# Kernel optimization log

Hardware: AMD Instinct MI355X
Metric: run time of the kernel (lower is better)

## Reference

```python
import jax, jax.numpy as jnp
import numpy as np


def conv(x, w, b=None, pad=1):
    y = jax.lax.conv_general_dilated(x, w, (1, 1), [(pad, pad), (pad, pad)],
                                     dimension_numbers=('NCHW', 'OIHW', 'NCHW'))
    if b is not None:
        y = y + b[None, :, None, None]
    return y


def grid_sample(img, gx, gy):
    # bilinear, zeros padding, align_corners=False (torch F.grid_sample default)
    B, C, H, W = img.shape
    ix = ((gx + 1.0) * W - 1.0) * 0.5
    iy = ((gy + 1.0) * H - 1.0) * 0.5
    x0 = jnp.floor(ix)
    y0 = jnp.floor(iy)

    def gather(xi, yi):
        valid = (xi >= 0) & (xi <= W - 1) & (yi >= 0) & (yi <= H - 1)
        xc = jnp.clip(xi, 0, W - 1).astype(jnp.int32)
        yc = jnp.clip(yi, 0, H - 1).astype(jnp.int32)
        b = jnp.arange(B)[:, None, None]
        return img[b, :, yc, xc] * valid[..., None].astype(img.dtype)  # (B,H,W,C)

    wx1 = ix - x0
    wy1 = iy - y0
    wx0 = 1.0 - wx1
    wy0 = 1.0 - wy1
    out = (gather(x0, y0) * (wx0 * wy0)[..., None]
           + gather(x0 + 1, y0) * (wx1 * wy0)[..., None]
           + gather(x0, y0 + 1) * (wx0 * wy1)[..., None]
           + gather(x0 + 1, y0 + 1) * (wx1 * wy1)[..., None])
    return out.transpose(0, 3, 1, 2)  # (B,C,H,W)


def setup_inputs() -> dict:
    key = jax.random.key(0)
    ks = jax.random.split(key, 32)
    B, H, W, hd = 4, 512, 512, 16
    f = lambda k, shp: jax.random.normal(k, shp, dtype=jnp.float32) * 0.05
    z = lambda n: jnp.zeros((n,), dtype=jnp.float32)
    d = {
        'net': f(ks[0], (B, hd, H, W)),
        'inp': f(ks[1], (B, hd, H, W)),
        'corr': f(ks[2], (B, 3, H, W)),
        'noise': f(ks[3], (B, 3, H, W)),
        # BasicMotionEncoder (channels=3, hidden=32, output_dim=64)
        'wc1': f(ks[4], (32, 3, 3, 3)), 'bc1': z(32),
        'wc2': f(ks[5], (32, 32, 3, 3)), 'bc2': z(32),
        'wf1': f(ks[6], (32, 3, 3, 3)), 'bf1': z(32),
        'wf2': f(ks[7], (32, 32, 3, 3)), 'bf2': z(32),
        'we': f(ks[8], (61, 64, 3, 3)), 'be': z(61),
        # SepConvGRU (hidden_size=16, L=4)
        'loc1_w': f(ks[9], (16, 96, 5, 5)), 'loc1_b': z(16),
        'loc2_w': f(ks[10], (8, 16, 5, 5)), 'loc2_b': z(8),
        'wz': f(ks[11], (16, 144, 3, 3)), 'bz': z(16),
        'wr': f(ks[12], (16, 144, 3, 3)), 'br': z(16),
        'wq': f(ks[13], (16, 96, 3, 3)), 'bq': z(16),
        # CBAM (reduction 16 -> mid=1; bias-free, standard impl)
        'ca_w1': f(ks[14], (1, 16, 1, 1)),
        'ca_w2': f(ks[15], (16, 1, 1, 1)),
        'sa_w': f(ks[16], (1, 2, 7, 7)),
        # FlowHead (input 16, hidden 64, out 3)
        'fh1_w': f(ks[17], (64, 16, 3, 3)), 'fh1_b': z(64),
        'fh2_w': f(ks[18], (3, 64, 3, 3)), 'fh2_b': z(3),
    }
    return d


def reference(net, inp, corr, noise, wc1, bc1, wc2, bc2, wf1, bf1, wf2, bf2, we, be,
              loc1_w, loc1_b, loc2_w, loc2_b, wz, bz, wr, br, wq, bq,
              ca_w1, ca_w2, sa_w, fh1_w, fh1_b, fh2_w, fh2_b):
    # --- BasicMotionEncoder ---
    cor = jax.nn.relu(conv(corr, wc1, bc1, 1))
    cor = jax.nn.relu(conv(cor, wc2, bc2, 1))
    flo = jax.nn.relu(conv(noise, wf1, bf1, 1))
    flo = jax.nn.relu(conv(flo, wf2, bf2, 1))
    mo = jax.nn.relu(conv(jnp.concatenate([cor, flo], 1), we, be, 1))
    motion = jnp.concatenate([mo, noise], 1)  # (B,64,H,W)
    x = jnp.concatenate([inp, motion], 1)     # (B,hd+64,H,W)
    h = net
    B, C, H, W = h.shape
    # --- SepConvGRU ---
    t = jax.nn.leaky_relu(conv(jnp.concatenate([x, h], 1), loc1_w, loc1_b, 2), 0.2)
    flows = conv(t, loc2_w, loc2_b, 2)        # (B,2L,H,W)
    L = flows.shape[1] // 2
    flows = flows.reshape(B, L, 2, H, W)
    xx = jnp.arange(W, dtype=h.dtype)[None, None, :]  # (1,1,W)
    yy = jnp.arange(H, dtype=h.dtype)[None, :, None]  # (1,H,1)

    def warp_one(flow):  # flow: (B,2,H,W); warp h by -flow
        vgx = xx - flow[:, 0]
        vgy = yy - flow[:, 1]
        gx = 2.0 * vgx / max(W - 1, 1) - 1.0
        gy = 2.0 * vgy / max(H - 1, 1) - 1.0
        return grid_sample(h, gx, gy)

    wrapped = jax.vmap(warp_one, in_axes=1, out_axes=1)(flows)  # (B,L,C,H,W)
    wrapped = wrapped.reshape(B, L * C, H, W)
    hx = jnp.concatenate([wrapped, x], 1)     # (B,9*hd,H,W)
    zg = jax.nn.sigmoid(conv(hx, wz, bz, 1))
    rg = jax.nn.sigmoid(conv(hx, wr, br, 1))
    q = jnp.tanh(conv(jnp.concatenate([rg * h, x], 1), wq, bq, 1))
    h = (1.0 - zg) * h + zg * q
    # --- CBAM ---
    avg = h.mean((2, 3), keepdims=True)
    mx = h.max((2, 3), keepdims=True)
    mlp = lambda v: conv(jax.nn.relu(conv(v, ca_w1, None, 0)), ca_w2, None, 0)
    h = h * jax.nn.sigmoid(mlp(avg) + mlp(mx))
    sa = jnp.concatenate([h.mean(1, keepdims=True), h.max(1, keepdims=True)], 1)
    h = h * jax.nn.sigmoid(conv(sa, sa_w, None, 3))
    # --- FlowHead ---
    delta_flow = conv(jax.nn.relu(conv(h, fh1_w, fh1_b, 1)), fh2_w, fh2_b, 1)
    return h, delta_flow
```

## Files before the change

kernel.cpp:

```cpp
#include <hip/hip_runtime.h>
#include <hip/hip_bf16.h>
#include <math.h>

using bf16 = __hip_bfloat16;
typedef __attribute__((ext_vector_type(8))) short short8;
typedef __attribute__((ext_vector_type(4))) float f32x4;

__device__ __forceinline__ float b2f(bf16 v){ return __bfloat162float(v); }
__device__ __forceinline__ bf16 f2b(float v){ return __float2bfloat16(v); }
__device__ __forceinline__ float bs2f(short s){
  union{unsigned u; float f;} x; x.u = ((unsigned)(unsigned short)s)<<16; return x.f;
}
__device__ __forceinline__ float lo16(unsigned u){ union{unsigned x; float f;} v; v.x = u<<16;          return v.f; }
__device__ __forceinline__ float hi16(unsigned u){ union{unsigned x; float f;} v; v.x = u & 0xffff0000u; return v.f; }
__device__ __forceinline__ unsigned cvt_pk_bf16(float lo, float hi){
  unsigned r; asm("v_cvt_pk_bf16_f32 %0, %1, %2" : "=v"(r) : "v"(lo), "v"(hi)); return r;
}
__device__ __forceinline__ float hw_exp2(float x){ float r; asm("v_exp_f32 %0, %1" : "=v"(r) : "v"(x)); return r; }
__device__ __forceinline__ float hw_rcp(float x){ float r; asm("v_rcp_f32 %0, %1" : "=v"(r) : "v"(x)); return r; }
__device__ __forceinline__ float fast_sigmoid(float v){ return hw_rcp(1.f + hw_exp2(v * -1.44269504f)); }
__device__ __forceinline__ float fast_tanh(float v){ return 1.f - 2.f*hw_rcp(1.f + hw_exp2(v * 2.88539008f)); }

template<int A> __device__ __forceinline__ float act_fn(float v){
  if constexpr (A==1) return fmaxf(v, 0.f);
  else if constexpr (A==2) return v > 0.f ? v : 0.2f*v;
  else if constexpr (A==3) return fast_sigmoid(v);
  else if constexpr (A==4) return fast_tanh(v);
  else return v;
}

struct Srcs9 { const bf16* p[9]; int code[9]; };

template<int KK, int ACT, int NT>
__global__ __launch_bounds__(256) void conv_mfma(
    Srcs9 S, int Gin, const bf16* __restrict__ flows, const bf16* __restrict__ rgp,
    const bf16* __restrict__ Bw, const float* __restrict__ bias,
    bf16* __restrict__ outS, size_t slabS, float* __restrict__ outF, int Cout,
    int H, int W)
{
  constexpr int TS=16, HALO=TS+KK-1, PAD=KK/2, NPAIR=(KK*KK+1)/2, HH=HALO*HALO;
  constexpr int CP=24, CPB=48;
  constexpr int NMT = (NT==1)?4:((NT==2)?8:16);
  __shared__ __align__(16) bf16 As[HH*CP];
  const int tid=threadIdx.x, lane=tid&63, wv=tid>>6;
  const int ln=lane&15, gq=lane>>4;
  const int tilesx=W/TS;
  const int nwg = gridDim.x, cpx = nwg >> 3;
  const int bidx = (blockIdx.x & 7)*cpx + (blockIdx.x >> 3);
  const int tx0 = (bidx % tilesx)*TS, ty0 = (bidx / tilesx)*TS;
  const int b=blockIdx.z; const int HW=H*W;
  int ntile, mt0;
  if constexpr (NT==1){ ntile=0;    mt0=wv*4; }
  else if constexpr (NT==2){ ntile=wv&1; mt0=(wv>>1)*8; }
  else { ntile=wv; mt0=0; }

  f32x4 acc[NMT];
  #pragma unroll
  for (int t=0;t<NMT;++t) acc[t]=(f32x4){0.f,0.f,0.f,0.f};

  const short8 Z8 = {0,0,0,0,0,0,0,0};
  const int px0=tid, px1=tid+256;
  const int hy0=px0/HALO, hx0=px0-hy0*HALO;
  const int hy1=px1/HALO, hx1=px1-hy1*HALO;
  const bool act1 = (px1<HH);
  const int gy0=ty0+hy0-PAD, gx0=tx0+hx0-PAD;
  const int gy1=ty0+hy1-PAD, gx1=tx0+hx1-PAD;
  const bool in0 = (gy0>=0&&gy0<H&&gx0>=0&&gx0<W);
  const bool in1 = act1 && (gy1>=0&&gy1<H&&gx1>=0&&gx1<W);
  const size_t po0 = ((size_t)b*HW + (size_t)(in0?gy0:0)*W + (in0?gx0:0))*16;
  const size_t po1 = ((size_t)b*HW + (size_t)(in1?gy1:0)*W + (in1?gx1:0))*16;

  auto gather = [&](int g, bool inb, size_t po, int gy, int gx, short8& A0, short8& A1){
    const int code = S.code[g];
    const bf16* sp = S.p[g];
    if (code == 0) {
      if (inb) {
        const bf16* qp = sp + po;
        A0 = *(const short8*)qp; A1 = *(const short8*)(qp+8);
      } else { A0 = Z8; A1 = Z8; }
    } else if (code == 5) {
      if (inb) {
        unsigned nu[8], ru[8], od[8];
        *(uint4*)nu     = *(const uint4*)(sp + po);  *(uint4*)(nu+4) = *(const uint4*)(sp + po + 8);
        *(uint4*)ru     = *(const uint4*)(rgp + po); *(uint4*)(ru+4) = *(const uint4*)(rgp + po + 8);
        #pragma unroll
        for (int j=0;j<8;++j)
          od[j] = cvt_pk_bf16(lo16(nu[j])*lo16(ru[j]), hi16(nu[j])*hi16(ru[j]));
        A0 = *(const short8*)od; A1 = *(const short8*)(od+4);
      } else { A0 = Z8; A1 = Z8; }
    } else {
      if (inb) {
        const int l = code-1;
        const unsigned fp_ = *(const unsigned*)(flows + po + 2*l);
        const float fx = lo16(fp_), fy = hi16(fp_);
        const float vgx = (float)gx - fx, vgy = (float)gy - fy;
        const float gxn = 2.f*vgx/(float)(W-1) - 1.f;
        const float gyn = 2.f*vgy/(float)(H-1) - 1.f;
        const float ix = ((gxn+1.f)*(float)W - 1.f)*0.5f;
        const float iy = ((gyn+1.f)*(float)H - 1.f)*0.5f;
        const float x0f = floorf(ix), y0f = floorf(iy);
        const float wx1 = ix-x0f, wy1 = iy-y0f, wx0 = 1.f-wx1, wy0 = 1.f-wy1;
        const int x0=(int)x0f, y0=(int)y0f, x1=x0+1, y1=y0+1;
        const bool vx0=(x0>=0)&(x0<W), vx1=(x1>=0)&(x1<W);
        const bool vy0=(y0>=0)&(y0<H), vy1=(y1>=0)&(y1<H);
        const int xc0=min(max(x0,0),W-1), xc1=min(max(x1,0),W-1);
        const int yc0=min(max(y0,0),H-1), yc1=min(max(y1,0),H-1);
        const float w00=wx0*wy0*((vx0&&vy0)?1.f:0.f);
        const float w10=wx1*wy0*((vx1&&vy0)?1.f:0.f);
        const float w01=wx0*wy1*((vx0&&vy1)?1.f:0.f);
        const float w11=wx1*wy1*((vx1&&vy1)?1.f:0.f);
        const bf16* nb = sp + (size_t)b*HW*16;
        const bf16* p00 = nb + ((size_t)yc0*W+xc0)*16;
        const bf16* p10 = nb + ((size_t)yc0*W+xc1)*16;
        const bf16* p01 = nb + ((size_t)yc1*W+xc0)*16;
        const bf16* p11 = nb + ((size_t)yc1*W+xc1)*16;
        unsigned t00[8], t10[8], t01[8], t11[8], od[8];
        *(uint4*)t00     = *(const uint4*)p00; *(uint4*)(t00+4) = *(const uint4*)(p00+8);
        *(uint4*)t10     = *(const uint4*)p10; *(uint4*)(t10+4) = *(const uint4*)(p10+8);
        *(uint4*)t01     = *(const uint4*)p01; *(uint4*)(t01+4) = *(const uint4*)(p01+8);
        *(uint4*)t11     = *(const uint4*)p11; *(uint4*)(t11+4) = *(const uint4*)(p11+8);
        #pragma unroll
        for (int j=0;j<8;++j){
          const float lo = w00*lo16(t00[j]) + w10*lo16(t10[j]) + w01*lo16(t01[j]) + w11*lo16(t11[j]);
          const float hi = w00*hi16(t00[j]) + w10*hi16(t10[j]) + w01*hi16(t01[j]) + w11*hi16(t11[j]);
          od[j] = cvt_pk_bf16(lo, hi);
        }
        A0 = *(const short8*)od; A1 = *(const short8*)(od+4);
      } else { A0 = Z8; A1 = Z8; }
    }
  };

  auto mfma_g = [&](int g){
    const bf16* bw = Bw + ((size_t)g*NPAIR*NT + ntile)*512;
    const char* bufm = (const char*)As + (size_t)mt0*(HALO*CPB);
    #pragma unroll
    for (int p=0;p<NPAIR;++p){
      const short8 bfrag = *(const short8*)(bw + (size_t)p*(NT*512) + lane*8);
      int off = 2*p + (gq>>1);
      if (off >= KK*KK) off = 0;
      const int dy = off/KK, dx = off - (off/KK)*KK;
      const int ce = (dy*HALO + ln + dx)*CPB + ((gq&1)<<4);
      #pragma unroll
      for (int t=0;t<NMT;++t){
        const short8 af = *(const short8*)(bufm + (size_t)t*(HALO*CPB) + ce);
        acc[t] = __builtin_amdgcn_mfma_f32_16x16x32_bf16(af, bfrag, acc[t], 0, 0, 0);
      }
    }
  };

  for (int g=0; g<Gin; ++g) {
    short8 a0, a1, c0v, c1v;
    gather(g, in0, po0, gy0, gx0, a0, a1);
    if (act1) gather(g, in1, po1, gy1, gx1, c0v, c1v);
    if (g > 0) { mfma_g(g-1); __syncthreads(); }
    *(short8*)(As + (size_t)px0*CP)     = a0;
    *(short8*)(As + (size_t)px0*CP + 8) = a1;
    if (act1){
      *(short8*)(As + (size_t)px1*CP)     = c0v;
      *(short8*)(As + (size_t)px1*CP + 8) = c1v;
    }
    __syncthreads();
  }
  mfma_g(Gin-1);

  const int co = ntile*16 + ln;
  const float bv = bias[co];
  if (outS) {
    #pragma unroll
    for (int t=0;t<NMT;++t){
      const int y = ty0 + mt0 + t;
      bf16* op = outS + (size_t)ntile*slabS + ((size_t)b*HW + (size_t)y*W + tx0 + gq*4)*16 + ln;
      const float f0 = act_fn<ACT>(acc[t][0] + bv);
      const float f1 = act_fn<ACT>(acc[t][1] + bv);
      const float f2 = act_fn<ACT>(acc[t][2] + bv);
      const float f3 = act_fn<ACT>(acc[t][3] + bv);
      const unsigned p01 = cvt_pk_bf16(f0, f1), p23 = cvt_pk_bf16(f2, f3);
      unsigned short* os = (unsigned short*)op;
      os[0]  = (unsigned short)p01; os[16] = (unsigned short)(p01>>16);
      os[32] = (unsigned short)p23; os[48] = (unsigned short)(p23>>16);
    }
  } else {
    if (co < Cout) {
      #pragma unroll
      for (int t=0;t<NMT;++t){
        const int y = ty0 + mt0 + t;
        float4 f;
        f.x = act_fn<ACT>(acc[t][0]+bv); f.y = act_fn<ACT>(acc[t][1]+bv);
        f.z = act_fn<ACT>(acc[t][2]+bv); f.w = act_fn<ACT>(acc[t][3]+bv);
        *(float4*)(outF + ((size_t)b*Cout + co)*HW + (size_t)y*W + tx0 + gq*4) = f;
      }
    }
  }
}

struct PrepDesc {
  const float *W1, *W2, *b1, *b2;
  int coSplit, NPAIR, NTp, Cout, CinO, T;
  int lo0, hi0, d2, lo2, hi2;
  int base[9];
  int total;
};
struct PrepAll { PrepDesc d[10]; int n; };

__device__ __forceinline__ void prep_body(const PrepAll& P, bf16* Bw, float* bOut,
                                          int grand, int i){
  if (i < P.n*64) {
    const int c=i>>6, t=i&63; const PrepDesc& D=P.d[c];
    float bv=0.f;
    if (t < D.Cout) bv = (!D.b2 || t < D.coSplit) ? D.b1[t] : D.b2[t-D.coSplit];
    bOut[c*64+t]=bv;
  }
  if (i >= grand) return;
  int c=0, off0=0;
  while (i >= off0 + P.d[c].total) { off0 += P.d[c].total; ++c; }
  const PrepDesc& D = P.d[c];
  const int j = i - off0;
  const int jj=j&7, l=(j>>3)&63, ln2=l&15, gq2=l>>4;
  int r=j>>9; const int nt=r%D.NTp; r/=D.NTp; const int p=r%D.NPAIR; const int g=r/D.NPAIR;
  const int k=gq2*8+jj, off=2*p+(k>>4), ci=k&15, co=nt*16+ln2;
  float w=0.f;
  if (off<D.T && co<D.Cout) {
    const int lo = (g==0)?D.lo0:0, hi=(g==0)?D.hi0:16;
    if (!D.W2 || co < D.coSplit) {
      if (ci>=lo && ci<hi) w = D.W1[((size_t)co*D.CinO + D.base[g]+ci)*D.T + off];
    } else {
      if (ci>=D.lo2 && ci<D.hi2) w = D.W2[((size_t)(co-D.coSplit)*D.CinO + D.base[g]+ci+D.d2)*D.T + off];
    }
  }
  Bw[i] = f2b(w);
}

__global__ void prep_w(PrepAll P, bf16* __restrict__ Bw, float* __restrict__ bOut, int grand){
  prep_body(P, Bw, bOut, grand, blockIdx.x*256 + threadIdx.x);
}

__global__ void prep_pack(PrepAll P, bf16* __restrict__ Bw, float* __restrict__ bOut, int grand,
                          const float* __restrict__ corr, const float* __restrict__ noise,
                          const float* __restrict__ inp, const float* __restrict__ net,
                          bf16* __restrict__ cnoise, bf16* __restrict__ inpT,
                          bf16* __restrict__ netT, int HW)
{
  const int b = blockIdx.y;
  if (b >= 4) { prep_body(P, Bw, bOut, grand, blockIdx.x*256 + threadIdx.x); return; }
  const int px = blockIdx.x*256+threadIdx.x;
  if (px>=HW) return;
  const size_t base = ((size_t)b*HW+px)*16;
  __align__(16) bf16 t[16];
  #pragma unroll
  for (int c=0;c<16;++c) t[c]=f2b(0.f);
  #pragma unroll
  for (int c=0;c<3;++c){
    t[c]   = f2b(corr [((size_t)b*3+c)*HW+px]);
    t[3+c] = f2b(noise[((size_t)b*3+c)*HW+px]);
  }
  *(short8*)(cnoise+base) = *(const short8*)t; *(short8*)(cnoise+base+8) = *(const short8*)(t+8);
  #pragma unroll
  for (int c=0;c<16;++c) t[c]=f2b(inp[((size_t)b*16+c)*HW+px]);
  *(short8*)(inpT+base) = *(const short8*)t; *(short8*)(inpT+base+8) = *(const short8*)(t+8);
  #pragma unroll
  for (int c=0;c<16;++c) t[c]=f2b(net[((size_t)b*16+c)*HW+px]);
  *(short8*)(netT+base) = *(const short8*)t; *(short8*)(netT+base+8) = *(const short8*)(t+8);
}

__global__ void noise_tail(const float* __restrict__ noise, bf16* __restrict__ mslab3, int HW){
  const int px = blockIdx.x*256+threadIdx.x; const int b=blockIdx.y;
  if (px>=HW) return;
  bf16* d = mslab3 + ((size_t)b*HW+px)*16;
  #pragma unroll
  for (int c=0;c<3;++c) d[13+c] = f2b(noise[((size_t)b*3+c)*HW+px]);
}

__global__ void h1_k(const bf16* __restrict__ zg, const bf16* __restrict__ q,
                     const bf16* __restrict__ netT, bf16* __restrict__ hT, int HW){
  const int px = blockIdx.x*256+threadIdx.x; const int b=blockIdx.y;
  if (px>=HW) return;
  const size_t base = ((size_t)b*HW+px)*16;
  const short8 z0=*(const short8*)(zg+base), z1=*(const short8*)(zg+base+8);
  const short8 q0=*(const short8*)(q+base),  q1=*(const short8*)(q+base+8);
  const short8 n0=*(const short8*)(netT+base), n1=*(const short8*)(netT+base+8);
  __align__(16) bf16 t[16];
  #pragma unroll
  for (int c=0;c<8;++c){
    const float za=bs2f(z0[c]), zb=bs2f(z1[c]);
    t[c]   = f2b((1.f-za)*bs2f(n0[c]) + za*bs2f(q0[c]));
    t[8+c] = f2b((1.f-zb)*bs2f(n1[c]) + zb*bs2f(q1[c]));
  }
  *(short8*)(hT+base) = *(const short8*)t; *(short8*)(hT+base+8) = *(const short8*)(t+8);
}

__global__ __launch_bounds__(256) void castats_p1(const bf16* __restrict__ hT,
                                                  float* __restrict__ part, int HW){
  const int blk=blockIdx.x, b=blockIdx.y;
  const int per = HW>>5;
  const bf16* base = hT + ((size_t)b*HW + (size_t)blk*per)*16;
  float s[16], m[16];
  #pragma unroll
  for (int c=0;c<16;++c){ s[c]=0.f; m[c]=-3.4e38f; }
  for (int i=threadIdx.x;i<per;i+=256){
    const short8 a=*(const short8*)(base+(size_t)i*16);
    const short8 bb=*(const short8*)(base+(size_t)i*16+8);
    #pragma unroll
    for (int c=0;c<8;++c){
      const float v=bs2f(a[c]);  s[c]+=v;   m[c]=fmaxf(m[c],v);
      const float w=bs2f(bb[c]); s[8+c]+=w; m[8+c]=fmaxf(m[8+c],w);
    }
  }
  #pragma unroll
  for (int o=32;o>=1;o>>=1){
    #pragma unroll
    for (int c=0;c<16;++c){ s[c]+=__shfl_down(s[c],o); m[c]=fmaxf(m[c],__shfl_down(m[c],o)); }
  }
  __shared__ float ls[4][16], lm[4][16];
  const int w4=threadIdx.x>>6;
  if ((threadIdx.x&63)==0){
    #pragma unroll
    for (int c=0;c<16;++c){ ls[w4][c]=s[c]; lm[w4][c]=m[c]; }
  }
  __syncthreads();
  if (threadIdx.x<16){
    const int c=threadIdx.x;
    part[((size_t)(b*32+blk))*32 + c]      = ls[0][c]+ls[1][c]+ls[2][c]+ls[3][c];
    part[((size_t)(b*32+blk))*32 + 16 + c] = fmaxf(fmaxf(lm[0][c],lm[1][c]),fmaxf(lm[2][c],lm[3][c]));
  }
}

__global__ void castats_fin(const float* __restrict__ part, const float* __restrict__ w1,
                            const float* __restrict__ w2, float* __restrict__ scale, int HW){
  const int t = threadIdx.x; if (t>=64) return;
  const int b=t>>4, c=t&15;
  float s=0.f, m=-3.4e38f;
  for (int k=0;k<32;++k){
    s += part[((size_t)(b*32+k))*32 + c];
    m  = fmaxf(m, part[((size_t)(b*32+k))*32 + 16 + c]);
  }
  float pa = w1[c]*(s/(float)HW), pm = w1[c]*m;
  #pragma unroll
  for (int o=8;o>=1;o>>=1){ pa += __shfl_xor(pa,o,16); pm += __shfl_xor(pm,o,16); }
  const float y = w2[c]*fmaxf(pa,0.f) + w2[c]*fmaxf(pm,0.f);
  scale[t] = fast_sigmoid(y);
}

__global__ void sastats_k(const bf16* __restrict__ hT, const float* __restrict__ scale,
                          bf16* __restrict__ sa2, int HW){
  const int px = blockIdx.x*256+threadIdx.x; const int b=blockIdx.y;
  if (px>=HW) return;
  const size_t base = ((size_t)b*HW+px)*16;
  const short8 a=*(const short8*)(hT+base), c8=*(const short8*)(hT+base+8);
  float s=0.f, m=-3.4e38f;
  #pragma unroll
  for (int c=0;c<8;++c){
    const float v=bs2f(a[c])*scale[b*16+c];    s+=v; m=fmaxf(m,v);
    const float w=bs2f(c8[c])*scale[b*16+8+c]; s+=w; m=fmaxf(m,w);
  }
  sa2[((size_t)b*2+0)*HW+px] = f2b(s*(1.f/16.f));
  sa2[((size_t)b*2+1)*HW+px] = f2b(m);
}

__global__ __launch_bounds__(256) void hfinal2(bf16* __restrict__ hT, const float* __restrict__ scale,
    const bf16* __restrict__ sa2, const float* __restrict__ saw,
    float* __restrict__ outh, int H, int W){
  __shared__ float wl[98];
  if (threadIdx.x < 98) wl[threadIdx.x] = saw[threadIdx.x];
  __syncthreads();
  const int i = blockIdx.x*256 + threadIdx.x; const int b = blockIdx.y;
  const int HW = H*W;
  if (i >= HW) return;
  const int y = i / W, x = i - (i/W)*W;
  float s = 0.f;
  #pragma unroll
  for (int ch=0; ch<2; ++ch){
    const size_t base = ((size_t)b*2+ch)*HW;
    for (int ky=0;ky<7;++ky){
      const int yy=y+ky-3; if (yy<0||yy>=H) continue;
      for (int kx=0;kx<7;++kx){
        const int xx=x+kx-3; if (xx<0||xx>=W) continue;
        s += b2f(sa2[base+(size_t)yy*W+xx]) * wl[ch*49+ky*7+kx];
      }
    }
  }
  const float sa = fast_sigmoid(s);
  const size_t base = ((size_t)b*HW+i)*16;
  const short8 a=*(const short8*)(hT+base), c8=*(const short8*)(hT+base+8);
  __align__(16) bf16 t[16];
  #pragma unroll
  for (int c=0;c<8;++c){
    const float v=bs2f(a[c])*scale[b*16+c]*sa;
    const float w=bs2f(c8[c])*scale[b*16+8+c]*sa;
    t[c]=f2b(v); t[8+c]=f2b(w);
    outh[((size_t)b*16+c)*HW+i]=v; outh[((size_t)b*16+8+c)*HW+i]=w;
  }
  *(short8*)(hT+base)=*(const short8*)t; *(short8*)(hT+base+8)=*(const short8*)(t+8);
}

extern "C" void kernel_launch(void* const* d_in, const int* in_sizes, int n_in,
                              void* d_out, int out_size, void* d_ws, size_t ws_size,
                              hipStream_t stream)
{
  const float* net   = (const float*)d_in[0];
  const float* inp   = (const float*)d_in[1];
  const float* corr  = (const float*)d_in[2];
  const float* noise = (const float*)d_in[3];
  const float* wc1 = (const float*)d_in[4];  const float* bc1 = (const float*)d_in[5];
  const float* wc2 = (const float*)d_in[6];  const float* bc2 = (const float*)d_in[7];
  const float* wf1 = (const float*)d_in[8];  const float* bf1 = (const float*)d_in[9];
  const float* wf2 = (const float*)d_in[10]; const float* bf2 = (const float*)d_in[11];
  const float* we  = (const float*)d_in[12]; const float* be  = (const float*)d_in[13];
  const float* loc1_w = (const float*)d_in[14]; const float* loc1_b = (const float*)d_in[15];
  const float* loc2_w = (const float*)d_in[16]; const float* loc2_b = (const float*)d_in[17];
  const float* wz = (const float*)d_in[18]; const float* bz = (const float*)d_in[19];
  const float* wr = (const float*)d_in[20]; const float* br = (const float*)d_in[21];
  const float* wq = (const float*)d_in[22]; const float* bq = (const float*)d_in[23];
  const float* ca_w1 = (const float*)d_in[24]; const float* ca_w2 = (const float*)d_in[25];
  const float* sa_w  = (const float*)d_in[26];
  const float* fh1_w = (const float*)d_in[27]; const float* fh1_b = (const float*)d_in[28];
  const float* fh2_w = (const float*)d_in[29]; const float* fh2_b = (const float*)d_in[30];

  const int B = 4, H = 512, W = 512, HW = H*W;
  const size_t U  = 32ull<<20;
  const size_t SS = (size_t)B*HW*16;
  char* ws = (char*)d_ws;

  bf16* cor1   = (bf16*)(ws + 0*U);
  bf16* flo1   = (bf16*)(ws + 2*U);
  bf16* motion = (bf16*)(ws + 0*U);
  bf16* fh1o   = (bf16*)(ws + 0*U);
  bf16* inpT   = (bf16*)(ws + 4*U);
  bf16* flo2   = (bf16*)(ws + 5*U);
  bf16* flows  = (bf16*)(ws + 5*U);
  bf16* qb     = (bf16*)(ws + 5*U);
  bf16* cnoise = (bf16*)(ws + 6*U);
  bf16* tbuf   = (bf16*)(ws + 6*U);
  bf16* hT     = (bf16*)(ws + 6*U);
  bf16* netT   = (bf16*)(ws + 7*U);
  float* part    = (float*)(ws + 4*U);
  float* scale   = (float*)(ws + 4*U + (64<<10));
  bf16*  sa2     = (bf16*)(ws + 4*U + (1<<20));
  bf16*  Bw_fh2  = (bf16*)(ws + 4*U + (16<<20));
  float* bias_fh2= (float*)(ws + 4*U + (17<<20));

  float* out_h  = (float*)d_out;
  float* out_df = out_h + (size_t)B*16*HW;
  bf16*  zgrg   = (bf16*)d_out;
  bf16*  BwAll  = (bf16*)out_df;
  float* biasAll= (float*)(BwAll + 190464);

  const size_t oMrg=0, oCor2=10240, oFlo2=20480, oMo=30720, oLoc1=71680,
               oLoc2=111616, oZgrg=118272, oQ=164352, oFh1=179712;
  const int grand = 189952;

  const dim3 pgrid((HW+255)/256, B);
  const dim3 cgrid((W/16)*(H/16), 1, B);

  auto mk = [](const float* W1, const float* W2, int coSplit, const float* b1, const float* b2,
               int G, int NP, int NTp, int Cout, int CinO, int T,
               int lo0, int hi0, int d2, int lo2, int hi2,
               int b0,int b1_,int b2_,int b3,int b4,int b5,int b6,int b7,int b8)->PrepDesc{
    PrepDesc d{};
    d.W1=W1; d.W2=W2; d.b1=b1; d.b2=b2; d.coSplit=coSplit;
    d.NPAIR=NP; d.NTp=NTp; d.Cout=Cout; d.CinO=CinO; d.T=T;
    d.lo0=lo0; d.hi0=hi0; d.d2=d2; d.lo2=lo2; d.hi2=hi2;
    const int bs[9]={b0,b1_,b2_,b3,b4,b5,b6,b7,b8};
    for (int g=0;g<9;++g) d.base[g]=bs[g];
    d.total = G*NP*NTp*512;
    return d;
  };

  {
    PrepAll P{}; P.n = 9;
    P.d[0] = mk(wc1, wf1, 32, bc1, bf1, 1,5,4, 64,3,9,  0,3, -3,3,6, 0,0,0,0,0,0,0,0,0);
    P.d[1] = mk(wc2, nullptr,0, bc2,nullptr, 2,5,2, 32,32,9, 0,16, 0,0,16, 0,16,0,0,0,0,0,0,0);
    P.d[2] = mk(wf2, nullptr,0, bf2,nullptr, 2,5,2, 32,32,9, 0,16, 0,0,16, 0,16,0,0,0,0,0,0,0);
    P.d[3] = mk(we,  nullptr,0, be, nullptr, 4,5,4, 61,64,9, 0,16, 0,0,16, 0,16,32,48,0,0,0,0,0);
    P.d[4] = mk(loc1_w,nullptr,0, loc1_b,nullptr, 6,13,1, 16,96,25, 0,16, 0,0,16, 0,16,32,48,64,80,0,0,0);
    P.d[5] = mk(loc2_w,nullptr,0, loc2_b,nullptr, 1,13,1, 8,16,25,  0,16, 0,0,16, 0,0,0,0,0,0,0,0,0);
    P.d[6] = mk(wz, wr, 16, bz, br, 9,5,2, 32,144,9, 0,16, 0,0,16, 0,16,32,48,64,80,96,112,128);
    P.d[7] = mk(wq, nullptr,0, bq, nullptr, 6,5,1, 16,96,9, 0,16, 0,0,16, 0,16,32,48,64,80,0,0,0);
    P.d[8] = mk(fh1_w,nullptr,0, fh1_b,nullptr, 1,5,4, 64,16,9, 0,16, 0,0,16, 0,0,0,0,0,0,0,0,0);
    prep_pack<<<dim3((HW+255)/256, B+1),256,0,stream>>>(P, BwAll, biasAll, grand,
        corr, noise, inp, net, cnoise, inpT, netT, HW);
  }

  { Srcs9 S{}; S.p[0]=cnoise;
    conv_mfma<3,1,4><<<cgrid,256,0,stream>>>(S,1,nullptr,nullptr,BwAll+oMrg,biasAll+0*64,cor1,SS,nullptr,64,H,W); }
  { Srcs9 S{}; S.p[0]=cor1; S.p[1]=cor1+SS;
    conv_mfma<3,1,2><<<cgrid,256,0,stream>>>(S,2,nullptr,nullptr,BwAll+oCor2,biasAll+1*64,zgrg,SS,nullptr,32,H,W); }
  { Srcs9 S{}; S.p[0]=flo1; S.p[1]=flo1+SS;
    conv_mfma<3,1,2><<<cgrid,256,0,stream>>>(S,2,nullptr,nullptr,BwAll+oFlo2,biasAll+2*64,flo2,SS,nullptr,32,H,W); }
  { Srcs9 S{}; S.p[0]=zgrg; S.p[1]=zgrg+SS; S.p[2]=flo2; S.p[3]=flo2+SS;
    conv_mfma<3,1,4><<<cgrid,256,0,stream>>>(S,4,nullptr,nullptr,BwAll+oMo,biasAll+3*64,motion,SS,nullptr,61,H,W); }
  noise_tail<<<pgrid,256,0,stream>>>(noise, motion+3*SS, HW);

  { Srcs9 S{}; S.p[0]=inpT; S.p[1]=motion; S.p[2]=motion+SS; S.p[3]=motion+2*SS; S.p[4]=motion+3*SS; S.p[5]=netT;
    conv_mfma<5,2,1><<<cgrid,256,0,stream>>>(S,6,nullptr,nullptr,BwAll+oLoc1,biasAll+4*64,tbuf,SS,nullptr,16,H,W); }
  { Srcs9 S{}; S.p[0]=tbuf;
    conv_mfma<5,0,1><<<cgrid,256,0,stream>>>(S,1,nullptr,nullptr,BwAll+oLoc2,biasAll+5*64,flows,SS,nullptr,8,H,W); }

  { Srcs9 S{};
    S.p[0]=netT; S.code[0]=1; S.p[1]=netT; S.code[1]=2;
    S.p[2]=netT; S.code[2]=3; S.p[3]=netT; S.code[3]=4;
    S.p[4]=inpT; S.p[5]=motion; S.p[6]=motion+SS; S.p[7]=motion+2*SS; S.p[8]=motion+3*SS;
    conv_mfma<3,3,2><<<cgrid,256,0,stream>>>(S,9,flows,nullptr,BwAll+oZgrg,biasAll+6*64,zgrg,SS,nullptr,32,H,W); }
  { Srcs9 S{};
    S.p[0]=netT; S.code[0]=5;
    S.p[1]=inpT; S.p[2]=motion; S.p[3]=motion+SS; S.p[4]=motion+2*SS; S.p[5]=motion+3*SS;
    conv_mfma<3,4,1><<<cgrid,256,0,stream>>>(S,6,nullptr,zgrg+SS,BwAll+oQ,biasAll+7*64,qb,SS,nullptr,16,H,W); }
  h1_k<<<pgrid,256,0,stream>>>(zgrg, qb, netT, hT, HW);

  { PrepAll P{}; P.n = 1;
    P.d[0] = mk(fh2_w,nullptr,0, fh2_b,nullptr, 4,5,1, 3,64,9, 0,16, 0,0,16, 0,16,32,48,0,0,0,0,0);
    prep_w<<<(10240+255)/256,256,0,stream>>>(P, Bw_fh2, bias_fh2, 10240); }

  castats_p1<<<dim3(32,B),256,0,stream>>>(hT, part, HW);
  castats_fin<<<1,64,0,stream>>>(part, ca_w1, ca_w2, scale, HW);
  sastats_k<<<pgrid,256,0,stream>>>(hT, scale, sa2, HW);
  hfinal2<<<pgrid,256,0,stream>>>(hT, scale, sa2, sa_w, out_h, H, W);

  { Srcs9 S{}; S.p[0]=hT;
    conv_mfma<3,1,4><<<cgrid,256,0,stream>>>(S,1,nullptr,nullptr,BwAll+oFh1,biasAll+8*64,fh1o,SS,nullptr,64,H,W); }
  { Srcs9 S{}; S.p[0]=fh1o; S.p[1]=fh1o+SS; S.p[2]=fh1o+2*SS; S.p[3]=fh1o+3*SS;
    conv_mfma<3,0,1><<<cgrid,256,0,stream>>>(S,4,nullptr,nullptr,Bw_fh2,bias_fh2,nullptr,SS,out_df,3,H,W); }
}
```

Before: 933.2 us.

## Fuse GRU update with CBAM channel stats and specialize rg-multiply gather path

The GRU output kernel now also computes per-block channel sums and maxes, which removes the separate castats pass that re-read hT. The finalize kernel is widened to reduce the larger number of partial blocks. Separately, a template flag compiles the r*h gather branch only into the q convolution, trimming branches and register pressure in the other conv instantiations. The trade-off is a per-pixel-block reduction with shuffles and barriers in the elementwise kernel, and a larger partial buffer.

```diff
diff --git a/kernel.cpp b/kernel.cpp
--- a/kernel.cpp
+++ b/kernel.cpp
@@ -31,7 +31,7 @@
 
 struct Srcs9 { const bf16* p[9]; int code[9]; };
 
-template<int KK, int ACT, int NT>
+template<int KK, int ACT, int NT, bool RG5=false>
 __global__ __launch_bounds__(256) void conv_mfma(
     Srcs9 S, int Gin, const bf16* __restrict__ flows, const bf16* __restrict__ rgp,
     const bf16* __restrict__ Bw, const float* __restrict__ bias,
@@ -78,17 +78,23 @@
         const bf16* qp = sp + po;
         A0 = *(const short8*)qp; A1 = *(const short8*)(qp+8);
       } else { A0 = Z8; A1 = Z8; }
-    } else if (code == 5) {
-      if (inb) {
-        unsigned nu[8], ru[8], od[8];
-        *(uint4*)nu     = *(const uint4*)(sp + po);  *(uint4*)(nu+4) = *(const uint4*)(sp + po + 8);
-        *(uint4*)ru     = *(const uint4*)(rgp + po); *(uint4*)(ru+4) = *(const uint4*)(rgp + po + 8);
-        #pragma unroll
-        for (int j=0;j<8;++j)
-          od[j] = cvt_pk_bf16(lo16(nu[j])*lo16(ru[j]), hi16(nu[j])*hi16(ru[j]));
-        A0 = *(const short8*)od; A1 = *(const short8*)(od+4);
-      } else { A0 = Z8; A1 = Z8; }
-    } else {
+      return;
+    }
+    if constexpr (RG5) {
+      if (code == 5) {
+        if (inb) {
+          unsigned nu[8], ru[8], od[8];
+          *(uint4*)nu     = *(const uint4*)(sp + po);  *(uint4*)(nu+4) = *(const uint4*)(sp + po + 8);
+          *(uint4*)ru     = *(const uint4*)(rgp + po); *(uint4*)(ru+4) = *(const uint4*)(rgp + po + 8);
+          #pragma unroll
+          for (int j=0;j<8;++j)
+            od[j] = cvt_pk_bf16(lo16(nu[j])*lo16(ru[j]), hi16(nu[j])*hi16(ru[j]));
+          A0 = *(const short8*)od; A1 = *(const short8*)(od+4);
+        } else { A0 = Z8; A1 = Z8; }
+        return;
+      }
+    }
+    {
       if (inb) {
         const int l = code-1;
         const unsigned fp_ = *(const unsigned*)(flows + po + 2*l);
@@ -270,41 +276,29 @@
   for (int c=0;c<3;++c) d[13+c] = f2b(noise[((size_t)b*3+c)*HW+px]);
 }
 
-__global__ void h1_k(const bf16* __restrict__ zg, const bf16* __restrict__ q,
-                     const bf16* __restrict__ netT, bf16* __restrict__ hT, int HW){
+__global__ __launch_bounds__(256) void h1_stats(const bf16* __restrict__ zg, const bf16* __restrict__ q,
+                     const bf16* __restrict__ netT, bf16* __restrict__ hT,
+                     float* __restrict__ part, int HW){
   const int px = blockIdx.x*256+threadIdx.x; const int b=blockIdx.y;
-  if (px>=HW) return;
   const size_t base = ((size_t)b*HW+px)*16;
   const short8 z0=*(const short8*)(zg+base), z1=*(const short8*)(zg+base+8);
   const short8 q0=*(const short8*)(q+base),  q1=*(const short8*)(q+base+8);
   const short8 n0=*(const short8*)(netT+base), n1=*(const short8*)(netT+base+8);
   __align__(16) bf16 t[16];
+  float v[16];
   #pragma unroll
   for (int c=0;c<8;++c){
     const float za=bs2f(z0[c]), zb=bs2f(z1[c]);
-    t[c]   = f2b((1.f-za)*bs2f(n0[c]) + za*bs2f(q0[c]));
-    t[8+c] = f2b((1.f-zb)*bs2f(n1[c]) + zb*bs2f(q1[c]));
+    const float a = (1.f-za)*bs2f(n0[c]) + za*bs2f(q0[c]);
+    const float d = (1.f-zb)*bs2f(n1[c]) + zb*bs2f(q1[c]);
+    v[c]=a; v[8+c]=d;
+    t[c]=f2b(a); t[8+c]=f2b(d);
   }
   *(short8*)(hT+base) = *(const short8*)t; *(short8*)(hT+base+8) = *(const short8*)(t+8);
-}
-
-__global__ __launch_bounds__(256) void castats_p1(const bf16* __restrict__ hT,
-                                                  float* __restrict__ part, int HW){
-  const int blk=blockIdx.x, b=blockIdx.y;
-  const int per = HW>>5;
-  const bf16* base = hT + ((size_t)b*HW + (size_t)blk*per)*16;
+
   float s[16], m[16];
   #pragma unroll
-  for (int c=0;c<16;++c){ s[c]=0.f; m[c]=-3.4e38f; }
-  for (int i=threadIdx.x;i<per;i+=256){
-    const short8 a=*(const short8*)(base+(size_t)i*16);
-    const short8 bb=*(const short8*)(base+(size_t)i*16+8);
-    #pragma unroll
-    for (int c=0;c<8;++c){
-      const float v=bs2f(a[c]);  s[c]+=v;   m[c]=fmaxf(m[c],v);
-      const float w=bs2f(bb[c]); s[8+c]+=w; m[8+c]=fmaxf(m[8+c],w);
-    }
-  }
+  for (int c=0;c<16;++c){ s[c]=v[c]; m[c]=v[c]; }
   #pragma unroll
   for (int o=32;o>=1;o>>=1){
     #pragma unroll
@@ -319,25 +313,42 @@
   __syncthreads();
   if (threadIdx.x<16){
     const int c=threadIdx.x;
-    part[((size_t)(b*32+blk))*32 + c]      = ls[0][c]+ls[1][c]+ls[2][c]+ls[3][c];
-    part[((size_t)(b*32+blk))*32 + 16 + c] = fmaxf(fmaxf(lm[0][c],lm[1][c]),fmaxf(lm[2][c],lm[3][c]));
-  }
-}
-
-__global__ void castats_fin(const float* __restrict__ part, const float* __restrict__ w1,
-                            const float* __restrict__ w2, float* __restrict__ scale, int HW){
-  const int t = threadIdx.x; if (t>=64) return;
-  const int b=t>>4, c=t&15;
+    float* pp = part + ((size_t)b*gridDim.x + blockIdx.x)*32;
+    pp[c]      = ls[0][c]+ls[1][c]+ls[2][c]+ls[3][c];
+    pp[16 + c] = fmaxf(fmaxf(lm[0][c],lm[1][c]),fmaxf(lm[2][c],lm[3][c]));
+  }
+}
+
+__global__ __launch_bounds__(256) void castats_fin(const float* __restrict__ part,
+                            const float* __restrict__ w1, const float* __restrict__ w2,
+                            float* __restrict__ scale, int HW, int nblk){
+  const int tid = threadIdx.x;
+  const int pair = tid >> 2, sub = tid & 3;
+  const int b = pair >> 4, c = pair & 15;
   float s=0.f, m=-3.4e38f;
-  for (int k=0;k<32;++k){
-    s += part[((size_t)(b*32+k))*32 + c];
-    m  = fmaxf(m, part[((size_t)(b*32+k))*32 + 16 + c]);
-  }
-  float pa = w1[c]*(s/(float)HW), pm = w1[c]*m;
-  #pragma unroll
-  for (int o=8;o>=1;o>>=1){ pa += __shfl_xor(pa,o,16); pm += __shfl_xor(pm,o,16); }
-  const float y = w2[c]*fmaxf(pa,0.f) + w2[c]*fmaxf(pm,0.f);
-  scale[t] = fast_sigmoid(y);
+  for (int k=sub; k<nblk; k+=4){
+    const float* p = part + ((size_t)b*nblk + k)*32;
+    s += p[c]; m = fmaxf(m, p[16+c]);
+  }
+  __shared__ float ls[256], lm[256];
+  ls[tid]=s; lm[tid]=m;
+  __syncthreads();
+  float s4=0.f, m4=-3.4e38f;
+  if (sub==0){
+    s4 = ls[tid]+ls[tid+1]+ls[tid+2]+ls[tid+3];
+    m4 = fmaxf(fmaxf(lm[tid],lm[tid+1]),fmaxf(lm[tid+2],lm[tid+3]));
+  }
+  __syncthreads();
+  if (sub==0){ ls[pair]=s4; lm[pair]=m4; }
+  __syncthreads();
+  if (tid < 64){
+    const int c2 = tid & 15;
+    float pa = w1[c2]*(ls[tid]/(float)HW), pm = w1[c2]*lm[tid];
+    #pragma unroll
+    for (int o=8;o>=1;o>>=1){ pa += __shfl_xor(pa,o,16); pm += __shfl_xor(pm,o,16); }
+    const float y = w2[c2]*fmaxf(pa,0.f) + w2[c2]*fmaxf(pm,0.f);
+    scale[tid] = fast_sigmoid(y);
+  }
 }
 
 __global__ void sastats_k(const bf16* __restrict__ hT, const float* __restrict__ scale,
@@ -433,7 +444,7 @@
   bf16* hT     = (bf16*)(ws + 6*U);
   bf16* netT   = (bf16*)(ws + 7*U);
   float* part    = (float*)(ws + 4*U);
-  float* scale   = (float*)(ws + 4*U + (64<<10));
+  float* scale   = (float*)(ws + 4*U + (640<<10));
   bf16*  sa2     = (bf16*)(ws + 4*U + (1<<20));
   bf16*  Bw_fh2  = (bf16*)(ws + 4*U + (16<<20));
   float* bias_fh2= (float*)(ws + 4*U + (17<<20));
@@ -503,15 +514,14 @@
   { Srcs9 S{};
     S.p[0]=netT; S.code[0]=5;
     S.p[1]=inpT; S.p[2]=motion; S.p[3]=motion+SS; S.p[4]=motion+2*SS; S.p[5]=motion+3*SS;
-    conv_mfma<3,4,1><<<cgrid,256,0,stream>>>(S,6,nullptr,zgrg+SS,BwAll+oQ,biasAll+7*64,qb,SS,nullptr,16,H,W); }
-  h1_k<<<pgrid,256,0,stream>>>(zgrg, qb, netT, hT, HW);
+    conv_mfma<3,4,1,true><<<cgrid,256,0,stream>>>(S,6,nullptr,zgrg+SS,BwAll+oQ,biasAll+7*64,qb,SS,nullptr,16,H,W); }
+  h1_stats<<<pgrid,256,0,stream>>>(zgrg, qb, netT, hT, part, HW);
 
   { PrepAll P{}; P.n = 1;
     P.d[0] = mk(fh2_w,nullptr,0, fh2_b,nullptr, 4,5,1, 3,64,9, 0,16, 0,0,16, 0,16,32,48,0,0,0,0,0);
     prep_w<<<(10240+255)/256,256,0,stream>>>(P, Bw_fh2, bias_fh2, 10240); }
 
-  castats_p1<<<dim3(32,B),256,0,stream>>>(hT, part, HW);
-  castats_fin<<<1,64,0,stream>>>(part, ca_w1, ca_w2, scale, HW);
+  castats_fin<<<1,256,0,stream>>>(part, ca_w1, ca_w2, scale, HW, (HW+255)/256);
   sastats_k<<<pgrid,256,0,stream>>>(hT, scale, sa2, HW);
   hfinal2<<<pgrid,256,0,stream>>>(hT, scale, sa2, sa_w, out_h, H, W);
 
```

After: 940.2 us. About the same (+0.7%).
